# Performance work log

Measured on AMD Instinct MI355X. Metric: run time of the kernel, lower is better.

## Reference

```python
import jax, jax.numpy as jnp
import numpy as np

N_NODES = 100000
N_EDGES = 1600000
D_FEAT = 64


def setup_inputs() -> dict:
    key = jax.random.key(0)
    k1, k2 = jax.random.split(key)
    x = jax.random.normal(k1, (N_NODES, D_FEAT), dtype=jnp.float32)
    edge_index = jax.random.randint(k2, (2, N_EDGES), 0, N_NODES, dtype=jnp.int64)
    alpha = jnp.ones((), dtype=jnp.float32)
    res_scale = jnp.ones((), dtype=jnp.float32)
    return {"x": x, "alpha": alpha, "res_scale": res_scale, "edge_index": edge_index}


def reference(x, alpha, res_scale, edge_index):
    """LGConv (symmetric gcn_norm, no self-loops) -> alpha-scale -> residual.

    out_i = alpha * sum_{(j->i) in E} x_j / sqrt(deg_i * deg_j) + res_scale * x_i
    """
    n = x.shape[0]
    row, col = edge_index[0], edge_index[1]  # source, target
    # degree from target index (as in PyG gcn_norm with add_self_loops=False)
    deg = jax.ops.segment_sum(jnp.ones(row.shape[0], dtype=x.dtype), col, num_segments=n)
    deg_inv_sqrt = jnp.where(deg > 0, jax.lax.rsqrt(jnp.maximum(deg, 1.0)), 0.0)
    norm = deg_inv_sqrt[row] * deg_inv_sqrt[col]  # (E,)
    msgs = norm[:, None] * x[row]                  # (E, d) gather + scale
    out = jax.ops.segment_sum(msgs, col, num_segments=n)  # scatter-add to targets
    return alpha * out + res_scale * x
```

## Files before the change

kernel.cpp:

```cpp
#include <hip/hip_runtime.h>
#include <hip/hip_bf16.h>

#define D_FEAT 64
#define OVF_CAP 65536
#define EB 4096
#define NBMAX 1024
#define CSL 32

typedef unsigned int uint32;

__device__ inline float blo(uint32 u) { return __uint_as_float(u << 16); }
__device__ inline float bhi(uint32 u) { return __uint_as_float(u & 0xffff0000u); }
__device__ inline float dinv(int d) { return (d > 0) ? rsqrtf((float)d) : 0.0f; }

__global__ __launch_bounds__(1024) void k_split(const int* __restrict__ row,
                                                const int* __restrict__ col,
                                                const float2* __restrict__ x2,
                                                uint32* __restrict__ xb,
                                                uint32* __restrict__ binned2,
                                                int* __restrict__ off,
                                                int nhalf, int E, int nb, int B) {
    __shared__ int    h[NBMAX];
    __shared__ int    P[1024];
    __shared__ uint32 st[EB];
    const int tid = threadIdx.x;
    const int b = blockIdx.x;
    for (int i = tid; i < nb; i += 1024) h[i] = 0;
    __syncthreads();
    const int s = b * EB;
    const int e = (s + EB < E) ? s + EB : E;
    for (int i = s + tid; i < e; i += 1024)
        atomicAdd(&h[col[i] >> 7], 1);
    __syncthreads();
    P[tid] = (tid < nb) ? h[tid] : 0;
    __syncthreads();
    for (int o = 1; o < 1024; o <<= 1) {
        int v = P[tid];
        if (tid >= o) v += P[tid - o];
        __syncthreads();
        P[tid] = v;
        __syncthreads();
    }
    int cntk = 0, excl = 0;
    if (tid < nb) { cntk = h[tid]; excl = P[tid] - cntk; }
    __syncthreads();
    if (tid < nb) {
        h[tid] = excl;
        off[(size_t)b * (nb + 1) + tid] = excl;
    }
    if (tid == 0) off[(size_t)b * (nb + 1) + nb] = e - s;
    __syncthreads();
    for (int i = s + tid; i < e; i += 1024) {
        int c = col[i];
        uint32 r = (uint32)row[i];
        int pos = atomicAdd(&h[c >> 7], 1);
        st[pos] = (r << 7) | (uint32)(c & 127);
    }
    __syncthreads();
    const int tot = e - s;
    uint32* dst = binned2 + (size_t)b * EB;
    for (int i = tid; i < tot; i += 1024) dst[i] = st[i];
    const int t = b * 1024 + tid;
    const int stride = B * 1024;
    for (int j = t; j < nhalf; j += stride) {
        float2 v = x2[j];
        __hip_bfloat16 bx = __float2bfloat16(v.x);
        __hip_bfloat16 by = __float2bfloat16(v.y);
        uint32 ux = *reinterpret_cast<unsigned short*>(&bx);
        uint32 uy = *reinterpret_cast<unsigned short*>(&by);
        xb[j] = ux | (uy << 16);
    }
}

__global__ __launch_bounds__(512) void k_build(const uint32* __restrict__ binned2,
                                               const int* __restrict__ off,
                                               int* __restrict__ slots,
                                               int* __restrict__ deg,
                                               float* __restrict__ winv,
                                               int2* __restrict__ ovf,
                                               int* __restrict__ ovf_cnt,
                                               int n, int nb, int B) {
    __shared__ int cnt[128];
    const int k = blockIdx.x;
    const int tid = threadIdx.x;
    if (tid < 128) cnt[tid] = 0;
    __syncthreads();
    const int base = k << 7;
    for (int b = tid; b < B; b += 512) {
        const int* ob = off + (size_t)b * (nb + 1) + k;
        int o0 = ob[0], o1 = ob[1];
        const uint32* sl = binned2 + (size_t)b * EB;
        for (int i = o0; i < o1; ++i) {
            uint32 pk = sl[i];
            int cl = (int)(pk & 127);
            int r  = (int)(pk >> 7);
            int rk = atomicAdd(&cnt[cl], 1);
            if (rk < CSL) {
                slots[(size_t)(base + cl) * CSL + rk] = r;
            } else {
                int o = atomicAdd(ovf_cnt, 1);
                if (o < OVF_CAP) ovf[o] = make_int2(r, base + cl);
            }
        }
    }
    __syncthreads();
    if (tid < 128) {
        int node = base + tid;
        if (node < n) {
            int d = cnt[tid];
            deg[node] = d;
            winv[node] = dinv(d);
        }
    }
}

__global__ void k_gather4d(const uint32* __restrict__ xb,
                           const float4* __restrict__ x4,
                           const int* __restrict__ deg,
                           const float* __restrict__ winv,
                           const int* __restrict__ slots,
                           const float* __restrict__ alpha_p,
                           const float* __restrict__ rs_p,
                           float4* __restrict__ out4, int n, int C) {
    int wid = (blockIdx.x * blockDim.x + threadIdx.x) >> 6;
    if (wid >= n) return;
    const int lane = threadIdx.x & 63;
    const int q = lane >> 4;
    const int l = lane & 15;
    int d = deg[wid];
    int e = (d < C) ? d : C;
    float4 xr = make_float4(0.f, 0.f, 0.f, 0.f);
    if (q == 0) xr = x4[(size_t)wid * 16 + l];
    const int* sl = slots + (size_t)wid * C;
    float ax = 0.f, ay = 0.f, az = 0.f, aw = 0.f;
    int k = 0;
    for (; k + 16 <= e; k += 16) {
        int s0 = sl[k + q];
        int s1 = sl[k + 4 + q];
        int s2 = sl[k + 8 + q];
        int s3 = sl[k + 12 + q];
        float w0 = winv[s0], w1 = winv[s1], w2 = winv[s2], w3 = winv[s3];
        uint2 p0 = ((const uint2*)(xb + (size_t)s0 * 32))[l];
        uint2 p1 = ((const uint2*)(xb + (size_t)s1 * 32))[l];
        uint2 p2 = ((const uint2*)(xb + (size_t)s2 * 32))[l];
        uint2 p3 = ((const uint2*)(xb + (size_t)s3 * 32))[l];
        ax = fmaf(w0, blo(p0.x), ax); ay = fmaf(w0, bhi(p0.x), ay);
        az = fmaf(w0, blo(p0.y), az); aw = fmaf(w0, bhi(p0.y), aw);
        ax = fmaf(w1, blo(p1.x), ax); ay = fmaf(w1, bhi(p1.x), ay);
        az = fmaf(w1, blo(p1.y), az); aw = fmaf(w1, bhi(p1.y), aw);
        ax = fmaf(w2, blo(p2.x), ax); ay = fmaf(w2, bhi(p2.x), ay);
        az = fmaf(w2, blo(p2.y), az); aw = fmaf(w2, bhi(p2.y), aw);
        ax = fmaf(w3, blo(p3.x), ax); ay = fmaf(w3, bhi(p3.x), ay);
        az = fmaf(w3, blo(p3.y), az); aw = fmaf(w3, bhi(p3.y), aw);
    }
    for (; k < e; k += 4) {
        int kk = k + q;
        if (kk < e) {
            int s0 = sl[kk];
            float w0 = winv[s0];
            uint2 p0 = ((const uint2*)(xb + (size_t)s0 * 32))[l];
            ax = fmaf(w0, blo(p0.x), ax); ay = fmaf(w0, bhi(p0.x), ay);
            az = fmaf(w0, blo(p0.y), az); aw = fmaf(w0, bhi(p0.y), aw);
        }
    }
    ax += __shfl_down(ax, 32, 64); ay += __shfl_down(ay, 32, 64);
    az += __shfl_down(az, 32, 64); aw += __shfl_down(aw, 32, 64);
    ax += __shfl_down(ax, 16, 64); ay += __shfl_down(ay, 16, 64);
    az += __shfl_down(az, 16, 64); aw += __shfl_down(aw, 16, 64);
    if (q == 0) {
        float adw = (*alpha_p) * winv[wid];
        float rs  = *rs_p;
        float4 o;
        o.x = fmaf(adw, ax, rs * xr.x);
        o.y = fmaf(adw, ay, rs * xr.y);
        o.z = fmaf(adw, az, rs * xr.z);
        o.w = fmaf(adw, aw, rs * xr.w);
        out4[(size_t)wid * 16 + l] = o;
    }
}

__global__ void k_ovf(const int2* __restrict__ ovf, const int* __restrict__ cnt_p,
                      const float* __restrict__ x, const float* __restrict__ winv,
                      const float* __restrict__ alpha_p, float* __restrict__ out) {
    int cnt = *cnt_p;
    if (cnt > OVF_CAP) cnt = OVF_CAP;
    if (cnt <= 0) return;
    float a = *alpha_p;
    long long total = (long long)cnt * 64;
    long long stride = (long long)gridDim.x * blockDim.x;
    for (long long idx = blockIdx.x * (long long)blockDim.x + threadIdx.x;
         idx < total; idx += stride) {
        int e = (int)(idx >> 6);
        int f = (int)(idx & 63);
        int2 rc = ovf[e];
        float w = a * winv[rc.x] * winv[rc.y];
        atomicAdd(&out[(size_t)rc.y * D_FEAT + f], w * x[(size_t)rc.x * D_FEAT + f]);
    }
}

__global__ void k_winv(const int* __restrict__ deg, float* __restrict__ winv, int n) {
    int i = blockIdx.x * blockDim.x + threadIdx.x;
    if (i < n) winv[i] = dinv(deg[i]);
}

__global__ __launch_bounds__(256) void k_prep(const float2* __restrict__ x2,
                                              uint32* __restrict__ xb,
                                              const int* __restrict__ row,
                                              const int* __restrict__ col,
                                              int* __restrict__ deg,
                                              int* __restrict__ slots,
                                              int2* __restrict__ ovf,
                                              int* __restrict__ ovf_cnt,
                                              int nhalf, int E, int C) {
    const int t = blockIdx.x * blockDim.x + threadIdx.x;
    if (t < E) {
        int c = col[t];
        int r = row[t];
        int rk = atomicAdd(&deg[c], 1);
        if (rk < C) {
            slots[(size_t)c * C + rk] = r;
        } else {
            int o = atomicAdd(ovf_cnt, 1);
            if (o < OVF_CAP) ovf[o] = make_int2(r, c);
        }
    }
    const int stride = gridDim.x * blockDim.x;
    for (int j = t; j < nhalf; j += stride) {
        float2 v = x2[j];
        __hip_bfloat16 bx = __float2bfloat16(v.x);
        __hip_bfloat16 by = __float2bfloat16(v.y);
        uint32 ux = *reinterpret_cast<unsigned short*>(&bx);
        uint32 uy = *reinterpret_cast<unsigned short*>(&by);
        xb[j] = ux | (uy << 16);
    }
}

static inline char* align_up(char* p, size_t a) {
    return (char*)(((uintptr_t)p + (a - 1)) & ~(uintptr_t)(a - 1));
}

extern "C" void kernel_launch(void* const* d_in, const int* in_sizes, int n_in,
                              void* d_out, int out_size, void* d_ws, size_t ws_size,
                              hipStream_t stream) {
    const float* x         = (const float*)d_in[0];
    const float* alpha     = (const float*)d_in[1];
    const float* res_scale = (const float*)d_in[2];
    const int*   ei        = (const int*)d_in[3];

    const int n = in_sizes[0] / D_FEAT;
    const int E = in_sizes[3] / 2;
    const int* row = ei;
    const int* col = ei + E;

    float* out = (float*)d_out;
    const int nhalf = n * (D_FEAT / 2);
    const int nb = (n + 127) >> 7;
    const int B  = (E + EB - 1) / EB;

    {
        char* p = (char*)d_ws;
        int*    deg     = (int*)p;            p += (size_t)n * 4;
        int*    ovf_cnt = (int*)p;            p += 4;
        float*  winv    = (float*)p;          p += (size_t)n * 4;
        int2*   ovf     = (int2*)p;           p += (size_t)OVF_CAP * 8;
        p = align_up(p, 16);
        uint32* xb      = (uint32*)p;         p += (size_t)n * 128;
        int*    slots   = (int*)p;            p += (size_t)n * CSL * 4;
        p = align_up(p, 16);
        uint32* binned2 = (uint32*)p;         p += (size_t)B * EB * 4;
        int*    off     = (int*)p;            p += (size_t)B * (nb + 1) * 4;
        const size_t need = (size_t)(p - (char*)d_ws);

        const bool ok = (need <= ws_size) && (nb <= NBMAX) && (n <= (NBMAX << 7));
        if (ok) {
            hipMemsetAsync(ovf_cnt, 0, 4, stream);
            k_split<<<B, 1024, 0, stream>>>(row, col, (const float2*)x, xb,
                                            binned2, off, nhalf, E, nb, B);
            k_build<<<nb, 512, 0, stream>>>(binned2, off, slots, deg, winv,
                                            ovf, ovf_cnt, n, nb, B);
            const long long tt = (long long)n * D_FEAT;
            const int blocks = (int)((tt + 255) / 256);
            k_gather4d<<<blocks, 256, 0, stream>>>(xb, (const float4*)x, deg, winv,
                                                   slots, alpha, res_scale,
                                                   (float4*)out, n, CSL);
            k_ovf<<<64, 256, 0, stream>>>(ovf, ovf_cnt, x, winv, alpha, out);
            return;
        }
    }

    {
        char* q = (char*)d_ws;
        int*    degf    = (int*)q;            q += (size_t)n * 4;
        int*    ovf_cf  = (int*)q;            q += 4;
        float*  winvf   = (float*)q;          q += (size_t)n * 4;
        int2*   ovff    = (int2*)q;           q += (size_t)OVF_CAP * 8;
        q = align_up(q, 16);
        uint32* xbf     = (uint32*)q;         q += (size_t)n * 128;
        int*    slotsf  = (int*)q;
        const size_t fxd = (size_t)(q - (char*)d_ws);
        int Cf = 0;
        if (ws_size > fxd) {
            size_t c_avail = (ws_size - fxd) / ((size_t)n * 4);
            Cf = (c_avail > 32) ? 32 : (int)c_avail;
        }
        if (Cf < 1) return;
        hipMemsetAsync(degf, 0, (size_t)n * 4 + 4, stream);
        k_prep<<<(E + 255) / 256, 256, 0, stream>>>(
            (const float2*)x, xbf, row, col, degf, slotsf, ovff, ovf_cf,
            nhalf, E, Cf);
        k_winv<<<(n + 255) / 256, 256, 0, stream>>>(degf, winvf, n);
        const long long tt = (long long)n * D_FEAT;
        const int blocks = (int)((tt + 255) / 256);
        k_gather4d<<<blocks, 256, 0, stream>>>(xbf, (const float4*)x, degf, winvf,
                                               slotsf, alpha, res_scale,
                                               (float4*)out, n, Cf);
        k_ovf<<<64, 256, 0, stream>>>(ovff, ovf_cf, x, winvf, alpha, out);
    }
}
```

Baseline: 190.9 us.

## Fuse slot building into gather using shared-memory slots per node bin

Splits the old build kernel into a degree-count pass and a fused kernel that rebuilds each 128-node bin's neighbor slot lists in shared memory and immediately gathers and writes outputs. This avoids writing and re-reading the global slots array (n*32 ints). It also replaces the memset of the overflow counter by zeroing it inside the split kernel. In exchange the binned edge list is scanned twice and the gather now runs with only 782 blocks of 8 waves each, with 16 nodes handled serially per wave, which may reduce latency hiding.

After: 194.2 us. About the same (+1.7%).

```diff
diff --git a/kernel.cpp b/kernel.cpp
--- a/kernel.cpp
+++ b/kernel.cpp
@@ -19,12 +19,14 @@
                                                 uint32* __restrict__ xb,
                                                 uint32* __restrict__ binned2,
                                                 int* __restrict__ off,
+                                                int* __restrict__ ovf_cnt,
                                                 int nhalf, int E, int nb, int B) {
     __shared__ int    h[NBMAX];
     __shared__ int    P[1024];
     __shared__ uint32 st[EB];
     const int tid = threadIdx.x;
     const int b = blockIdx.x;
+    if (b == 0 && tid == 0) *ovf_cnt = 0;
     for (int i = tid; i < nb; i += 1024) h[i] = 0;
     __syncthreads();
     const int s = b * EB;
@@ -72,15 +74,48 @@
     }
 }
 
-__global__ __launch_bounds__(512) void k_build(const uint32* __restrict__ binned2,
+__global__ __launch_bounds__(512) void k_count(const uint32* __restrict__ binned2,
                                                const int* __restrict__ off,
-                                               int* __restrict__ slots,
                                                int* __restrict__ deg,
                                                float* __restrict__ winv,
-                                               int2* __restrict__ ovf,
-                                               int* __restrict__ ovf_cnt,
                                                int n, int nb, int B) {
     __shared__ int cnt[128];
+    const int k = blockIdx.x;
+    const int tid = threadIdx.x;
+    if (tid < 128) cnt[tid] = 0;
+    __syncthreads();
+    for (int b = tid; b < B; b += 512) {
+        const int* ob = off + (size_t)b * (nb + 1) + k;
+        int o0 = ob[0], o1 = ob[1];
+        const uint32* sl = binned2 + (size_t)b * EB;
+        for (int i = o0; i < o1; ++i)
+            atomicAdd(&cnt[(int)(sl[i] & 127)], 1);
+    }
+    __syncthreads();
+    if (tid < 128) {
+        int node = (k << 7) + tid;
+        if (node < n) {
+            int d = cnt[tid];
+            deg[node] = d;
+            winv[node] = dinv(d);
+        }
+    }
+}
+
+__global__ __launch_bounds__(512) void k_rgather(const uint32* __restrict__ binned2,
+                                                 const int* __restrict__ off,
+                                                 const float* __restrict__ winv,
+                                                 const uint32* __restrict__ xb,
+                                                 const float4* __restrict__ x4,
+                                                 const float* __restrict__ alpha_p,
+                                                 const float* __restrict__ rs_p,
+                                                 float4* __restrict__ out4,
+                                                 int2* __restrict__ ovf,
+                                                 int* __restrict__ ovf_cnt,
+                                                 int n, int nb, int B) {
+    __shared__ int   slots[128 * CSL];
+    __shared__ int   cnt[128];
+    __shared__ float winvl[128];
     const int k = blockIdx.x;
     const int tid = threadIdx.x;
     if (tid < 128) cnt[tid] = 0;
@@ -96,7 +131,7 @@
             int r  = (int)(pk >> 7);
             int rk = atomicAdd(&cnt[cl], 1);
             if (rk < CSL) {
-                slots[(size_t)(base + cl) * CSL + rk] = r;
+                slots[(cl << 5) + rk] = r;
             } else {
                 int o = atomicAdd(ovf_cnt, 1);
                 if (o < OVF_CAP) ovf[o] = make_int2(r, base + cl);
@@ -106,11 +141,124 @@
     __syncthreads();
     if (tid < 128) {
         int node = base + tid;
-        if (node < n) {
-            int d = cnt[tid];
-            deg[node] = d;
-            winv[node] = dinv(d);
-        }
+        winvl[tid] = (node < n) ? winv[node] : 0.f;
+    }
+    __syncthreads();
+
+    const int wv   = tid >> 6;
+    const int lane = tid & 63;
+    const int q = lane >> 4;
+    const int l = lane & 15;
+    const float alpha = *alpha_p;
+    const float rs = *rs_p;
+    for (int nl = (wv << 4); nl < (wv << 4) + 16; ++nl) {
+        int node = base + nl;
+        if (node >= n) break;
+        int e = cnt[nl];
+        if (e > CSL) e = CSL;
+        float4 xr = make_float4(0.f, 0.f, 0.f, 0.f);
+        if (q == 0) xr = x4[(size_t)node * 16 + l];
+        const int* sl = &slots[nl << 5];
+        float ax = 0.f, ay = 0.f, az = 0.f, aw = 0.f;
+        int kk = 0;
+        for (; kk + 16 <= e; kk += 16) {
+            int s0 = sl[kk + q];
+            int s1 = sl[kk + 4 + q];
+            int s2 = sl[kk + 8 + q];
+            int s3 = sl[kk + 12 + q];
+            float w0 = winv[s0], w1 = winv[s1], w2 = winv[s2], w3 = winv[s3];
+            uint2 p0 = ((const uint2*)(xb + (size_t)s0 * 32))[l];
+            uint2 p1 = ((const uint2*)(xb + (size_t)s1 * 32))[l];
+            uint2 p2 = ((const uint2*)(xb + (size_t)s2 * 32))[l];
+            uint2 p3 = ((const uint2*)(xb + (size_t)s3 * 32))[l];
+            ax = fmaf(w0, blo(p0.x), ax); ay = fmaf(w0, bhi(p0.x), ay);
+            az = fmaf(w0, blo(p0.y), az); aw = fmaf(w0, bhi(p0.y), aw);
+            ax = fmaf(w1, blo(p1.x), ax); ay = fmaf(w1, bhi(p1.x), ay);
+            az = fmaf(w1, blo(p1.y), az); aw = fmaf(w1, bhi(p1.y), aw);
+            ax = fmaf(w2, blo(p2.x), ax); ay = fmaf(w2, bhi(p2.x), ay);
+            az = fmaf(w2, blo(p2.y), az); aw = fmaf(w2, bhi(p2.y), aw);
+            ax = fmaf(w3, blo(p3.x), ax); ay = fmaf(w3, bhi(p3.x), ay);
+            az = fmaf(w3, blo(p3.y), az); aw = fmaf(w3, bhi(p3.y), aw);
+        }
+        for (; kk < e; kk += 4) {
+            int ki = kk + q;
+            if (ki < e) {
+                int s0 = sl[ki];
+                float w0 = winv[s0];
+                uint2 p0 = ((const uint2*)(xb + (size_t)s0 * 32))[l];
+                ax = fmaf(w0, blo(p0.x), ax); ay = fmaf(w0, bhi(p0.x), ay);
+                az = fmaf(w0, blo(p0.y), az); aw = fmaf(w0, bhi(p0.y), aw);
+            }
+        }
+        ax += __shfl_down(ax, 32, 64); ay += __shfl_down(ay, 32, 64);
+        az += __shfl_down(az, 32, 64); aw += __shfl_down(aw, 32, 64);
+        ax += __shfl_down(ax, 16, 64); ay += __shfl_down(ay, 16, 64);
+        az += __shfl_down(az, 16, 64); aw += __shfl_down(aw, 16, 64);
+        if (q == 0) {
+            float adw = alpha * winvl[nl];
+            float4 o;
+            o.x = fmaf(adw, ax, rs * xr.x);
+            o.y = fmaf(adw, ay, rs * xr.y);
+            o.z = fmaf(adw, az, rs * xr.z);
+            o.w = fmaf(adw, aw, rs * xr.w);
+            out4[(size_t)node * 16 + l] = o;
+        }
+    }
+}
+
+__global__ void k_ovf(const int2* __restrict__ ovf, const int* __restrict__ cnt_p,
+                      const float* __restrict__ x, const float* __restrict__ winv,
+                      const float* __restrict__ alpha_p, float* __restrict__ out) {
+    int cnt = *cnt_p;
+    if (cnt > OVF_CAP) cnt = OVF_CAP;
+    if (cnt <= 0) return;
+    float a = *alpha_p;
+    long long total = (long long)cnt * 64;
+    long long stride = (long long)gridDim.x * blockDim.x;
+    for (long long idx = blockIdx.x * (long long)blockDim.x + threadIdx.x;
+         idx < total; idx += stride) {
+        int e = (int)(idx >> 6);
+        int f = (int)(idx & 63);
+        int2 rc = ovf[e];
+        float w = a * winv[rc.x] * winv[rc.y];
+        atomicAdd(&out[(size_t)rc.y * D_FEAT + f], w * x[(size_t)rc.x * D_FEAT + f]);
+    }
+}
+
+__global__ void k_winv(const int* __restrict__ deg, float* __restrict__ winv, int n) {
+    int i = blockIdx.x * blockDim.x + threadIdx.x;
+    if (i < n) winv[i] = dinv(deg[i]);
+}
+
+__global__ __launch_bounds__(256) void k_prep(const float2* __restrict__ x2,
+                                              uint32* __restrict__ xb,
+                                              const int* __restrict__ row,
+                                              const int* __restrict__ col,
+                                              int* __restrict__ deg,
+                                              int* __restrict__ slots,
+                                              int2* __restrict__ ovf,
+                                              int* __restrict__ ovf_cnt,
+                                              int nhalf, int E, int C) {
+    const int t = blockIdx.x * blockDim.x + threadIdx.x;
+    if (t < E) {
+        int c = col[t];
+        int r = row[t];
+        int rk = atomicAdd(&deg[c], 1);
+        if (rk < C) {
+            slots[(size_t)c * C + rk] = r;
+        } else {
+            int o = atomicAdd(ovf_cnt, 1);
+            if (o < OVF_CAP) ovf[o] = make_int2(r, c);
+        }
+    }
+    const int stride = gridDim.x * blockDim.x;
+    for (int j = t; j < nhalf; j += stride) {
+        float2 v = x2[j];
+        __hip_bfloat16 bx = __float2bfloat16(v.x);
+        __hip_bfloat16 by = __float2bfloat16(v.y);
+        uint32 ux = *reinterpret_cast<unsigned short*>(&bx);
+        uint32 uy = *reinterpret_cast<unsigned short*>(&by);
+        xb[j] = ux | (uy << 16);
     }
 }
 
@@ -179,62 +327,6 @@
     }
 }
 
-__global__ void k_ovf(const int2* __restrict__ ovf, const int* __restrict__ cnt_p,
-                      const float* __restrict__ x, const float* __restrict__ winv,
-                      const float* __restrict__ alpha_p, float* __restrict__ out) {
-    int cnt = *cnt_p;
-    if (cnt > OVF_CAP) cnt = OVF_CAP;
-    if (cnt <= 0) return;
-    float a = *alpha_p;
-    long long total = (long long)cnt * 64;
-    long long stride = (long long)gridDim.x * blockDim.x;
-    for (long long idx = blockIdx.x * (long long)blockDim.x + threadIdx.x;
-         idx < total; idx += stride) {
-        int e = (int)(idx >> 6);
-        int f = (int)(idx & 63);
-        int2 rc = ovf[e];
-        float w = a * winv[rc.x] * winv[rc.y];
-        atomicAdd(&out[(size_t)rc.y * D_FEAT + f], w * x[(size_t)rc.x * D_FEAT + f]);
-    }
-}
-
-__global__ void k_winv(const int* __restrict__ deg, float* __restrict__ winv, int n) {
-    int i = blockIdx.x * blockDim.x + threadIdx.x;
-    if (i < n) winv[i] = dinv(deg[i]);
-}
-
-__global__ __launch_bounds__(256) void k_prep(const float2* __restrict__ x2,
-                                              uint32* __restrict__ xb,
-                                              const int* __restrict__ row,
-                                              const int* __restrict__ col,
-                                              int* __restrict__ deg,
-                                              int* __restrict__ slots,
-                                              int2* __restrict__ ovf,
-                                              int* __restrict__ ovf_cnt,
-                                              int nhalf, int E, int C) {
-    const int t = blockIdx.x * blockDim.x + threadIdx.x;
-    if (t < E) {
-        int c = col[t];
-        int r = row[t];
-        int rk = atomicAdd(&deg[c], 1);
-        if (rk < C) {
-            slots[(size_t)c * C + rk] = r;
-        } else {
-            int o = atomicAdd(ovf_cnt, 1);
-            if (o < OVF_CAP) ovf[o] = make_int2(r, c);
-        }
-    }
-    const int stride = gridDim.x * blockDim.x;
-    for (int j = t; j < nhalf; j += stride) {
-        float2 v = x2[j];
-        __hip_bfloat16 bx = __float2bfloat16(v.x);
-        __hip_bfloat16 by = __float2bfloat16(v.y);
-        uint32 ux = *reinterpret_cast<unsigned short*>(&bx);
-        uint32 uy = *reinterpret_cast<unsigned short*>(&by);
-        xb[j] = ux | (uy << 16);
-    }
-}
-
 static inline char* align_up(char* p, size_t a) {
     return (char*)(((uintptr_t)p + (a - 1)) & ~(uintptr_t)(a - 1));
 }
@@ -265,7 +357,6 @@
         int2*   ovf     = (int2*)p;           p += (size_t)OVF_CAP * 8;
         p = align_up(p, 16);
         uint32* xb      = (uint32*)p;         p += (size_t)n * 128;
-        int*    slots   = (int*)p;            p += (size_t)n * CSL * 4;
         p = align_up(p, 16);
         uint32* binned2 = (uint32*)p;         p += (size_t)B * EB * 4;
         int*    off     = (int*)p;            p += (size_t)B * (nb + 1) * 4;
@@ -273,16 +364,13 @@
 
         const bool ok = (need <= ws_size) && (nb <= NBMAX) && (n <= (NBMAX << 7));
         if (ok) {
-            hipMemsetAsync(ovf_cnt, 0, 4, stream);
             k_split<<<B, 1024, 0, stream>>>(row, col, (const float2*)x, xb,
-                                            binned2, off, nhalf, E, nb, B);
-            k_build<<<nb, 512, 0, stream>>>(binned2, off, slots, deg, winv,
-                                            ovf, ovf_cnt, n, nb, B);
-            const long long tt = (long long)n * D_FEAT;
-            const int blocks = (int)((tt + 255) / 256);
-            k_gather4d<<<blocks, 256, 0, stream>>>(xb, (const float4*)x, deg, winv,
-                                                   slots, alpha, res_scale,
-                                                   (float4*)out, n, CSL);
+                                            binned2, off, ovf_cnt,
+                                            nhalf, E, nb, B);
+            k_count<<<nb, 512, 0, stream>>>(binned2, off, deg, winv, n, nb, B);
+            k_rgather<<<nb, 512, 0, stream>>>(binned2, off, winv, xb,
+                                              (const float4*)x, alpha, res_scale,
+                                              (float4*)out, ovf, ovf_cnt, n, nb, B);
             k_ovf<<<64, 256, 0, stream>>>(ovf, ovf_cnt, x, winv, alpha, out);
             return;
         }
```
